# Optimization experiments

Measured on AMD Instinct MI355X. Metric: run time of the kernel, lower is better.

Reference implementation:

```python
import jax, jax.numpy as jnp
import numpy as np

T, B, D, H = 512, 64, 512, 512


def lstm_cell(x, h, c, Wih, Whh, bih, bhh):
    # PyTorch LSTMCell: gates = x @ Wih.T + h @ Whh.T + bih + bhh, order [i, f, g, o]
    gates = x @ Wih.T + h @ Whh.T + (bih + bhh)
    i, f, g, o = jnp.split(gates, 4, axis=-1)
    i = jax.nn.sigmoid(i)
    f = jax.nn.sigmoid(f)
    g = jnp.tanh(g)
    o = jax.nn.sigmoid(o)
    c_new = f * c + i * g
    h_new = o * jnp.tanh(c_new)
    return h_new, c_new


def setup_inputs() -> dict:
    key = jax.random.key(0)
    ks = jax.random.split(key, 10)
    scale = 1.0 / np.sqrt(H)
    x_data = jax.random.normal(ks[0], (T, B, D), dtype=jnp.float32)
    # realistic padding mask: sorted lengths per batch element (mask[t, b] = t < len_b)
    lengths = jax.random.randint(ks[1], (B,), T // 2, T + 1)
    x_mask = (jnp.arange(T)[:, None] < lengths[None, :]).astype(jnp.float32)
    def unif(k, shape):
        return jax.random.uniform(k, shape, jnp.float32, -scale, scale)
    params = {
        'Wih_f': unif(ks[2], (4 * H, D)), 'Whh_f': unif(ks[3], (4 * H, H)),
        'bih_f': unif(ks[4], (4 * H,)),   'bhh_f': unif(ks[5], (4 * H,)),
        'Wih_r': unif(ks[6], (4 * H, D)), 'Whh_r': unif(ks[7], (4 * H, H)),
        'bih_r': unif(ks[8], (4 * H,)),   'bhh_r': unif(ks[9], (4 * H,)),
    }
    return {'x_data': x_data, 'x_mask': x_mask, **params}


def reference(x_data, x_mask, Wih_f, Whh_f, bih_f, bhh_f, Wih_r, Whh_r, bih_r, bhh_r):
    # x_data: [T, B, D], x_mask: [T, B]
    x_rev = x_data[::-1]
    m_rev = x_mask[::-1]

    def step(carry, inp):
        hf, cf, hr, cr = carry
        xf, xr, mf, mr = inp
        hf2, cf2 = lstm_cell(xf, hf, cf, Wih_f, Whh_f, bih_f, bhh_f)
        hr2, cr2 = lstm_cell(xr, hr, cr, Wih_r, Whh_r, bih_r, bhh_r)
        mf_ = mf[:, None]
        mr_ = mr[:, None]
        hf = hf2 * mf_ + hf * (1.0 - mf_)
        cf = cf2 * mf_ + cf * (1.0 - mf_)
        hr = hr2 * mr_ + hr * (1.0 - mr_)
        cr = cr2 * mr_ + cr * (1.0 - mr_)
        return (hf, cf, hr, cr), (hf, hr)

    z = jnp.zeros((B, H), dtype=x_data.dtype)
    _, (out_f, out_r) = jax.lax.scan(step, (z, z, z, z), (x_data, x_rev, x_mask, m_rev))
    # reverse outputs of the backward direction (original inserts at front)
    return jnp.concatenate([out_f, out_r[::-1]], axis=2)  # [T, B, 2H]
```

## Files before the change

### kernel.cpp

```cpp
#include <hip/hip_runtime.h>
#include <hip/hip_cooperative_groups.h>
#include <math.h>

namespace cg = cooperative_groups;

namespace {
constexpr int T = 512, B = 64, D = 512, H = 512;
constexpr int WROW = 1028;
constexpr int CHK  = 128;
constexpr int XROW = 132;
constexpr int WLDS = 16 * WROW;
constexpr int XLDS = 2 * B * XROW;
constexpr int PROW = 36;
}

__global__ __launch_bounds__(512, 2) void bilstm_persistent(
    const float* __restrict__ x, const float* __restrict__ mask,
    const float* __restrict__ WihF, const float* __restrict__ WhhF,
    const float* __restrict__ bihF, const float* __restrict__ bhhF,
    const float* __restrict__ WihR, const float* __restrict__ WhhR,
    const float* __restrict__ bihR, const float* __restrict__ bhhR,
    float* __restrict__ hbuf, float* __restrict__ out)
{
  cg::grid_group grid = cg::this_grid();
  __shared__ float smem[WLDS + XLDS];
  float* const wlds = smem;
  float* const xh   = smem + WLDS;
  float* const P    = smem + WLDS;

  const int tid = threadIdx.x;
  const int dir = (int)blockIdx.x >> 7;
  const int j0  = ((int)blockIdx.x & 127) * 4;

  const float* __restrict__ Wih = dir ? WihR : WihF;
  const float* __restrict__ Whh = dir ? WhhR : WhhF;
  const float* __restrict__ bih = dir ? bihR : bihF;
  const float* __restrict__ bhh = dir ? bhhR : bhhF;

  for (int idx = tid; idx < 16 * 256; idx += 512) {
    const int row = idx >> 8, f4 = idx & 255;
    const int g = row >> 2, jj = row & 3;
    const int k = f4 * 4;
    const float* src = (k < D)
        ? Wih + (size_t)(g * H + j0 + jj) * D + k
        : Whh + (size_t)(g * H + j0 + jj) * H + (k - D);
    *(float4*)&wlds[row * WROW + k] = *(const float4*)src;
  }

  const int fb = tid & 63, fjj = tid >> 6;
  float bs0 = 0.f, bs1 = 0.f, bs2 = 0.f, bs3 = 0.f, cReg = 0.f, hReg = 0.f;
  if (tid < 256) {
    bs0 = bih[0 * H + j0 + fjj] + bhh[0 * H + j0 + fjj];
    bs1 = bih[1 * H + j0 + fjj] + bhh[1 * H + j0 + fjj];
    bs2 = bih[2 * H + j0 + fjj] + bhh[2 * H + j0 + fjj];
    bs3 = bih[3 * H + j0 + fjj] + bhh[3 * H + j0 + fjj];
    hbuf[((size_t)dir * B + fb) * H + j0 + fjj] = 0.f;
  }

  const int bq  = tid & 15;
  const int jjc = (tid >> 4) & 3;
  const int kq  = tid >> 6;

  float4 gx0, gx1, gx2, gx3;
  const int sb = tid >> 5, sf4 = tid & 31;

  auto issue_chunk = [&](int c, int s) {
    const int t = dir ? (T - 1 - s) : s;
    const float* src = (c < 4)
        ? x + (size_t)t * B * D + c * CHK
        : hbuf + ((size_t)((s & 1) * 2 + dir) * B) * H + (c * CHK - D);
    src += (size_t)sb * 512 + sf4 * 4;
    gx0 = *(const float4*)(src);
    gx1 = *(const float4*)(src + 16 * 512);
    gx2 = *(const float4*)(src + 32 * 512);
    gx3 = *(const float4*)(src + 48 * 512);
  };
  auto write_chunk = [&](int c) {
    float* dst = xh + (c & 1) * (B * XROW) + sb * XROW + sf4 * 4;
    *(float4*)(dst)             = gx0;
    *(float4*)(dst + 16 * XROW) = gx1;
    *(float4*)(dst + 32 * XROW) = gx2;
    *(float4*)(dst + 48 * XROW) = gx3;
  };

  issue_chunk(0, 0);
  grid.sync();

  for (int s = 0; s < T; ++s) {
    float acc[4][4];
    #pragma unroll
    for (int i = 0; i < 4; ++i)
      #pragma unroll
      for (int g = 0; g < 4; ++g) acc[i][g] = 0.f;

    #pragma unroll 2
    for (int c = 0; c < 8; ++c) {
      __syncthreads();
      write_chunk(c);
      if (c < 7) issue_chunk(c + 1, s);
      __syncthreads();
      const float* wb = wlds + jjc * WROW + c * CHK + kq * 16;
      const float* xb = xh + (c & 1) * (B * XROW) + kq * 16;
      #pragma unroll
      for (int k4 = 0; k4 < 4; ++k4) {
        const int ko = k4 * 4;
        float4 w0 = *(const float4*)(wb + 0 * 4 * WROW + ko);
        float4 w1 = *(const float4*)(wb + 1 * 4 * WROW + ko);
        float4 w2 = *(const float4*)(wb + 2 * 4 * WROW + ko);
        float4 w3 = *(const float4*)(wb + 3 * 4 * WROW + ko);
        #pragma unroll
        for (int i = 0; i < 4; ++i) {
          float4 hv = *(const float4*)(xb + (bq + 16 * i) * XROW + ko);
          acc[i][0] += hv.x * w0.x + hv.y * w0.y + hv.z * w0.z + hv.w * w0.w;
          acc[i][1] += hv.x * w1.x + hv.y * w1.y + hv.z * w1.z + hv.w * w1.w;
          acc[i][2] += hv.x * w2.x + hv.y * w2.y + hv.z * w2.z + hv.w * w2.w;
          acc[i][3] += hv.x * w3.x + hv.y * w3.y + hv.z * w3.z + hv.w * w3.w;
        }
      }
    }

    __syncthreads();
    #pragma unroll
    for (int i = 0; i < 4; ++i)
      #pragma unroll
      for (int g = 0; g < 4; ++g)
        P[((bq + 16 * i) * 4 + jjc) * PROW + g * 8 + kq] = acc[i][g];
    __syncthreads();

    if (tid < 256) {
      const float* pr = P + (fb * 4 + fjj) * PROW;
      float s0 = bs0, s1 = bs1, s2 = bs2, s3 = bs3;
      #pragma unroll
      for (int g4 = 0; g4 < 2; ++g4) {
        float4 a0 = *(const float4*)(pr + 0 * 8 + g4 * 4);
        float4 a1 = *(const float4*)(pr + 1 * 8 + g4 * 4);
        float4 a2 = *(const float4*)(pr + 2 * 8 + g4 * 4);
        float4 a3 = *(const float4*)(pr + 3 * 8 + g4 * 4);
        s0 += a0.x + a0.y + a0.z + a0.w;
        s1 += a1.x + a1.y + a1.z + a1.w;
        s2 += a2.x + a2.y + a2.z + a2.w;
        s3 += a3.x + a3.y + a3.z + a3.w;
      }
      const int t = dir ? (T - 1 - s) : s;
      const float ig = 1.f / (1.f + expf(-s0));
      const float fg = 1.f / (1.f + expf(-s1));
      const float gg = tanhf(s2);
      const float og = 1.f / (1.f + expf(-s3));
      const float cNew = fg * cReg + ig * gg;
      const float hNew = og * tanhf(cNew);
      const float m = mask[(size_t)t * B + fb];
      hReg = hNew * m + hReg * (1.f - m);
      cReg = cNew * m + cReg * (1.f - m);
      hbuf[((size_t)(((s + 1) & 1) * 2 + dir) * B + fb) * H + j0 + fjj] = hReg;
      out[((size_t)t * B + fb) * (2 * H) + (size_t)dir * H + j0 + fjj] = hReg;
    }
    if (s + 1 < T) issue_chunk(0, s + 1);
    grid.sync();
  }
}

extern "C" void kernel_launch(void* const* d_in, const int* in_sizes, int n_in,
                              void* d_out, int out_size, void* d_ws, size_t ws_size,
                              hipStream_t stream) {
  const float* x    = (const float*)d_in[0];
  const float* mask = (const float*)d_in[1];
  const float* WihF = (const float*)d_in[2];
  const float* WhhF = (const float*)d_in[3];
  const float* bihF = (const float*)d_in[4];
  const float* bhhF = (const float*)d_in[5];
  const float* WihR = (const float*)d_in[6];
  const float* WhhR = (const float*)d_in[7];
  const float* bihR = (const float*)d_in[8];
  const float* bhhR = (const float*)d_in[9];
  float* hbuf = (float*)d_ws;
  float* outp = (float*)d_out;

  void* args[] = {(void*)&x, (void*)&mask,
                  (void*)&WihF, (void*)&WhhF, (void*)&bihF, (void*)&bhhF,
                  (void*)&WihR, (void*)&WhhR, (void*)&bihR, (void*)&bhhR,
                  (void*)&hbuf, (void*)&outp};
  hipLaunchCooperativeKernel((const void*)bilstm_persistent,
                             dim3(256), dim3(512), args, 0, stream);
}
```

Before: 22.62 ms.

## Rewrite BiLSTM step with split-bf16 MFMA, register weights, per-direction counters

```diff
diff --git a/kernel.cpp b/kernel.cpp
--- a/kernel.cpp
+++ b/kernel.cpp
@@ -1,161 +1,197 @@
 #include <hip/hip_runtime.h>
-#include <hip/hip_cooperative_groups.h>
+#include <hip/hip_bf16.h>
 #include <math.h>
 
-namespace cg = cooperative_groups;
+typedef __attribute__((ext_vector_type(8))) short bf16x8;
+typedef __attribute__((ext_vector_type(4))) float f32x4;
+typedef __attribute__((ext_vector_type(4))) unsigned u32x4;
 
 namespace {
 constexpr int T = 512, B = 64, D = 512, H = 512;
-constexpr int WROW = 1028;
-constexpr int CHK  = 128;
-constexpr int XROW = 132;
-constexpr int WLDS = 16 * WROW;
-constexpr int XLDS = 2 * B * XROW;
-constexpr int PROW = 36;
-}
-
-__global__ __launch_bounds__(512, 2) void bilstm_persistent(
+constexpr int NBLK = 128;
+constexpr int PLANE = B * H;
+constexpr int XPOFF = 4096;
+}
+
+__global__ __launch_bounds__(64) void ws_init(int* cnt) {
+  if (threadIdx.x < 16) cnt[threadIdx.x] = 0;
+}
+
+static __device__ __forceinline__ f32x4 mfma16(bf16x8 a, bf16x8 b, f32x4 c) {
+  return __builtin_amdgcn_mfma_f32_16x16x32_bf16(a, b, c, 0, 0, 0);
+}
+
+static __device__ __forceinline__ void split2(float v0, float v1,
+                                              unsigned& hi, unsigned& lo) {
+  unsigned b0 = __builtin_bit_cast(unsigned, v0);
+  unsigned b1 = __builtin_bit_cast(unsigned, v1);
+  hi = (b0 >> 16) | (b1 & 0xffff0000u);
+  float r0 = v0 - __builtin_bit_cast(float, b0 & 0xffff0000u);
+  float r1 = v1 - __builtin_bit_cast(float, b1 & 0xffff0000u);
+  lo = (__builtin_bit_cast(unsigned, r0) >> 16) |
+       (__builtin_bit_cast(unsigned, r1) & 0xffff0000u);
+}
+static __device__ __forceinline__ void split8(float4 a, float4 b,
+                                              bf16x8& hi8, bf16x8& lo8) {
+  unsigned h0, h1, h2, h3, l0, l1, l2, l3;
+  split2(a.x, a.y, h0, l0); split2(a.z, a.w, h1, l1);
+  split2(b.x, b.y, h2, l2); split2(b.z, b.w, h3, l3);
+  u32x4 uh = {h0, h1, h2, h3}, ul = {l0, l1, l2, l3};
+  hi8 = __builtin_bit_cast(bf16x8, uh);
+  lo8 = __builtin_bit_cast(bf16x8, ul);
+}
+
+__global__ __launch_bounds__(512, 2) void bilstm_mfma(
     const float* __restrict__ x, const float* __restrict__ mask,
     const float* __restrict__ WihF, const float* __restrict__ WhhF,
     const float* __restrict__ bihF, const float* __restrict__ bhhF,
     const float* __restrict__ WihR, const float* __restrict__ WhhR,
     const float* __restrict__ bihR, const float* __restrict__ bhhR,
-    float* __restrict__ hbuf, float* __restrict__ out)
+    unsigned short* __restrict__ hpl, int* __restrict__ cnt,
+    float* __restrict__ out)
 {
-  cg::grid_group grid = cg::this_grid();
-  __shared__ float smem[WLDS + XLDS];
-  float* const wlds = smem;
-  float* const xh   = smem + WLDS;
-  float* const P    = smem + WLDS;
-
-  const int tid = threadIdx.x;
-  const int dir = (int)blockIdx.x >> 7;
-  const int j0  = ((int)blockIdx.x & 127) * 4;
+  __shared__ float P[XPOFF + 2 * 4096];
+
+  const int tid  = threadIdx.x;
+  const int dir  = (int)blockIdx.x >> 7;
+  const int j0   = ((int)blockIdx.x & 127) * 4;
+  const int wave = tid >> 6, lane = tid & 63;
+  const int q = lane >> 4, ln15 = lane & 15;
+  const bool is_h = wave >= 4;
+  const int wh = wave - 4;
 
   const float* __restrict__ Wih = dir ? WihR : WihF;
   const float* __restrict__ Whh = dir ? WhhR : WhhF;
   const float* __restrict__ bih = dir ? bihR : bihF;
   const float* __restrict__ bhh = dir ? bhhR : bhhF;
 
-  for (int idx = tid; idx < 16 * 256; idx += 512) {
-    const int row = idx >> 8, f4 = idx & 255;
-    const int g = row >> 2, jj = row & 3;
-    const int k = f4 * 4;
-    const float* src = (k < D)
-        ? Wih + (size_t)(g * H + j0 + jj) * D + k
-        : Whh + (size_t)(g * H + j0 + jj) * H + (k - D);
-    *(float4*)&wlds[row * WROW + k] = *(const float4*)src;
-  }
-
-  const int fb = tid & 63, fjj = tid >> 6;
+  const int jj = ln15 >> 2, g = ln15 & 3;
+
+  bf16x8 Whi[4], Wlo[4];
+  {
+    const float* Wm  = is_h ? Whh : Wih;
+    const int kb     = (is_h ? wh : wave) * 128;
+    const float* wr  = Wm + (size_t)(g * H + j0 + jj) * 512 + kb;
+    #pragma unroll
+    for (int ks = 0; ks < 4; ++ks) {
+      const float* p = wr + ks * 32 + q * 8;
+      split8(*(const float4*)p, *(const float4*)(p + 4), Whi[ks], Wlo[ks]);
+    }
+  }
+
+  const int fb = (tid >> 2) & 63, fjj = tid & 3;
   float bs0 = 0.f, bs1 = 0.f, bs2 = 0.f, bs3 = 0.f, cReg = 0.f, hReg = 0.f;
   if (tid < 256) {
     bs0 = bih[0 * H + j0 + fjj] + bhh[0 * H + j0 + fjj];
     bs1 = bih[1 * H + j0 + fjj] + bhh[1 * H + j0 + fjj];
     bs2 = bih[2 * H + j0 + fjj] + bhh[2 * H + j0 + fjj];
     bs3 = bih[3 * H + j0 + fjj] + bhh[3 * H + j0 + fjj];
-    hbuf[((size_t)dir * B + fb) * H + j0 + fjj] = 0.f;
-  }
-
-  const int bq  = tid & 15;
-  const int jjc = (tid >> 4) & 3;
-  const int kq  = tid >> 6;
-
-  float4 gx0, gx1, gx2, gx3;
-  const int sb = tid >> 5, sf4 = tid & 31;
-
-  auto issue_chunk = [&](int c, int s) {
-    const int t = dir ? (T - 1 - s) : s;
-    const float* src = (c < 4)
-        ? x + (size_t)t * B * D + c * CHK
-        : hbuf + ((size_t)((s & 1) * 2 + dir) * B) * H + (c * CHK - D);
-    src += (size_t)sb * 512 + sf4 * 4;
-    gx0 = *(const float4*)(src);
-    gx1 = *(const float4*)(src + 16 * 512);
-    gx2 = *(const float4*)(src + 32 * 512);
-    gx3 = *(const float4*)(src + 48 * 512);
+  }
+
+  auto x_gemm = [&](int t, int par) {
+    f32x4 acc[4] = {{0,0,0,0},{0,0,0,0},{0,0,0,0},{0,0,0,0}};
+    #pragma unroll
+    for (int mt = 0; mt < 4; ++mt) {
+      const float* xr = x + ((size_t)t * B + ln15 + 16 * mt) * D + wave * 128 + q * 8;
+      #pragma unroll
+      for (int ks = 0; ks < 4; ++ks) {
+        bf16x8 Ah, Al;
+        split8(*(const float4*)(xr + ks * 32),
+               *(const float4*)(xr + ks * 32 + 4), Ah, Al);
+        acc[mt] = mfma16(Ah, Whi[ks], acc[mt]);
+        acc[mt] = mfma16(Ah, Wlo[ks], acc[mt]);
+        acc[mt] = mfma16(Al, Whi[ks], acc[mt]);
+      }
+    }
+    float* dst = P + XPOFF + par * 4096 + wave * 1024;
+    #pragma unroll
+    for (int mt = 0; mt < 4; ++mt)
+      #pragma unroll
+      for (int r = 0; r < 4; ++r)
+        dst[mt * 256 + (q * 4 + r) * 16 + ln15] = acc[mt][r];
   };
-  auto write_chunk = [&](int c) {
-    float* dst = xh + (c & 1) * (B * XROW) + sb * XROW + sf4 * 4;
-    *(float4*)(dst)             = gx0;
-    *(float4*)(dst + 16 * XROW) = gx1;
-    *(float4*)(dst + 32 * XROW) = gx2;
-    *(float4*)(dst + 48 * XROW) = gx3;
+
+  auto h_gemm = [&](int s) {
+    const unsigned short* phi =
+        hpl + ((size_t)((s & 1) * 2 + dir) * 2) * PLANE;
+    const unsigned short* plo = phi + PLANE;
+    f32x4 acc[4] = {{0,0,0,0},{0,0,0,0},{0,0,0,0},{0,0,0,0}};
+    #pragma unroll
+    for (int mt = 0; mt < 4; ++mt) {
+      const size_t base = (size_t)(ln15 + 16 * mt) * H + wh * 128 + q * 8;
+      #pragma unroll
+      for (int ks = 0; ks < 4; ++ks) {
+        bf16x8 Ah = *(const bf16x8*)(phi + base + ks * 32);
+        bf16x8 Al = *(const bf16x8*)(plo + base + ks * 32);
+        acc[mt] = mfma16(Ah, Whi[ks], acc[mt]);
+        acc[mt] = mfma16(Ah, Wlo[ks], acc[mt]);
+        acc[mt] = mfma16(Al, Whi[ks], acc[mt]);
+      }
+    }
+    float* dst = P + wh * 1024;
+    #pragma unroll
+    for (int mt = 0; mt < 4; ++mt)
+      #pragma unroll
+      for (int r = 0; r < 4; ++r)
+        dst[mt * 256 + (q * 4 + r) * 16 + ln15] = acc[mt][r];
   };
 
-  issue_chunk(0, 0);
-  grid.sync();
+  if (is_h) {
+    for (int i = tid - 256; i < 4096; i += 256) P[i] = 0.f;
+  } else {
+    x_gemm(dir ? (T - 1) : 0, 0);
+  }
 
   for (int s = 0; s < T; ++s) {
-    float acc[4][4];
-    #pragma unroll
-    for (int i = 0; i < 4; ++i)
-      #pragma unroll
-      for (int g = 0; g < 4; ++g) acc[i][g] = 0.f;
-
-    #pragma unroll 2
-    for (int c = 0; c < 8; ++c) {
-      __syncthreads();
-      write_chunk(c);
-      if (c < 7) issue_chunk(c + 1, s);
-      __syncthreads();
-      const float* wb = wlds + jjc * WROW + c * CHK + kq * 16;
-      const float* xb = xh + (c & 1) * (B * XROW) + kq * 16;
-      #pragma unroll
-      for (int k4 = 0; k4 < 4; ++k4) {
-        const int ko = k4 * 4;
-        float4 w0 = *(const float4*)(wb + 0 * 4 * WROW + ko);
-        float4 w1 = *(const float4*)(wb + 1 * 4 * WROW + ko);
-        float4 w2 = *(const float4*)(wb + 2 * 4 * WROW + ko);
-        float4 w3 = *(const float4*)(wb + 3 * 4 * WROW + ko);
-        #pragma unroll
-        for (int i = 0; i < 4; ++i) {
-          float4 hv = *(const float4*)(xb + (bq + 16 * i) * XROW + ko);
-          acc[i][0] += hv.x * w0.x + hv.y * w0.y + hv.z * w0.z + hv.w * w0.w;
-          acc[i][1] += hv.x * w1.x + hv.y * w1.y + hv.z * w1.z + hv.w * w1.w;
-          acc[i][2] += hv.x * w2.x + hv.y * w2.y + hv.z * w2.z + hv.w * w2.w;
-          acc[i][3] += hv.x * w3.x + hv.y * w3.y + hv.z * w3.z + hv.w * w3.w;
-        }
-      }
-    }
-
+    if (is_h) {
+      if (s > 0) {
+        const int target = NBLK * s;
+        while (__hip_atomic_load(&cnt[dir], __ATOMIC_RELAXED,
+                                 __HIP_MEMORY_SCOPE_AGENT) < target)
+          __builtin_amdgcn_s_sleep(2);
+        __threadfence();
+        h_gemm(s);
+      }
+    } else {
+      if (s + 1 < T) x_gemm(dir ? (T - 2 - s) : (s + 1), (s + 1) & 1);
+    }
     __syncthreads();
-    #pragma unroll
-    for (int i = 0; i < 4; ++i)
-      #pragma unroll
-      for (int g = 0; g < 4; ++g)
-        P[((bq + 16 * i) * 4 + jjc) * PROW + g * 8 + kq] = acc[i][g];
-    __syncthreads();
 
     if (tid < 256) {
-      const float* pr = P + (fb * 4 + fjj) * PROW;
-      float s0 = bs0, s1 = bs1, s2 = bs2, s3 = bs3;
-      #pragma unroll
-      for (int g4 = 0; g4 < 2; ++g4) {
-        float4 a0 = *(const float4*)(pr + 0 * 8 + g4 * 4);
-        float4 a1 = *(const float4*)(pr + 1 * 8 + g4 * 4);
-        float4 a2 = *(const float4*)(pr + 2 * 8 + g4 * 4);
-        float4 a3 = *(const float4*)(pr + 3 * 8 + g4 * 4);
-        s0 += a0.x + a0.y + a0.z + a0.w;
-        s1 += a1.x + a1.y + a1.z + a1.w;
-        s2 += a2.x + a2.y + a2.z + a2.w;
-        s3 += a3.x + a3.y + a3.z + a3.w;
-      }
       const int t = dir ? (T - 1 - s) : s;
-      const float ig = 1.f / (1.f + expf(-s0));
-      const float fg = 1.f / (1.f + expf(-s1));
-      const float gg = tanhf(s2);
-      const float og = 1.f / (1.f + expf(-s3));
+      const float mval = mask[(size_t)t * B + fb];
+      const int off = (fb >> 4) * 256 + (fb & 15) * 16 + fjj * 4;
+      const float* xPr = P + XPOFF + (s & 1) * 4096;
+      f32x4 sum = {bs0, bs1, bs2, bs3};
+      #pragma unroll
+      for (int w = 0; w < 4; ++w) {
+        sum += *(const f32x4*)(P + w * 1024 + off);
+        sum += *(const f32x4*)(xPr + w * 1024 + off);
+      }
+      const float ig = 1.f / (1.f + expf(-sum[0]));
+      const float fg = 1.f / (1.f + expf(-sum[1]));
+      const float gg = tanhf(sum[2]);
+      const float og = 1.f / (1.f + expf(-sum[3]));
       const float cNew = fg * cReg + ig * gg;
       const float hNew = og * tanhf(cNew);
-      const float m = mask[(size_t)t * B + fb];
-      hReg = hNew * m + hReg * (1.f - m);
-      cReg = cNew * m + cReg * (1.f - m);
-      hbuf[((size_t)(((s + 1) & 1) * 2 + dir) * B + fb) * H + j0 + fjj] = hReg;
+      hReg = hNew * mval + hReg * (1.f - mval);
+      cReg = cNew * mval + cReg * (1.f - mval);
+
+      unsigned hb = __builtin_bit_cast(unsigned, hReg);
+      unsigned short hhi = (unsigned short)(hb >> 16);
+      float rres = hReg - __builtin_bit_cast(float, hb & 0xffff0000u);
+      unsigned short hlo =
+          (unsigned short)(__builtin_bit_cast(unsigned, rres) >> 16);
+      unsigned short* nh =
+          hpl + ((size_t)((((s + 1) & 1) * 2 + dir)) * 2) * PLANE +
+          (size_t)fb * H + j0 + fjj;
+      nh[0] = hhi;
+      nh[PLANE] = hlo;
       out[((size_t)t * B + fb) * (2 * H) + (size_t)dir * H + j0 + fjj] = hReg;
-    }
-    if (s + 1 < T) issue_chunk(0, s + 1);
-    grid.sync();
+      __threadfence();
+    }
+    __syncthreads();
+    if (tid == 0 && s + 1 < T) atomicAdd(&cnt[dir], 1);
   }
 }
 
@@ -172,13 +208,17 @@
   const float* WhhR = (const float*)d_in[7];
   const float* bihR = (const float*)d_in[8];
   const float* bhhR = (const float*)d_in[9];
-  float* hbuf = (float*)d_ws;
   float* outp = (float*)d_out;
+
+  int* cnt = (int*)d_ws;
+  unsigned short* hpl = (unsigned short*)((char*)d_ws + 64);
+
+  ws_init<<<1, 64, 0, stream>>>(cnt);
 
   void* args[] = {(void*)&x, (void*)&mask,
                   (void*)&WihF, (void*)&WhhF, (void*)&bihF, (void*)&bhhF,
                   (void*)&WihR, (void*)&WhhR, (void*)&bihR, (void*)&bhhR,
-                  (void*)&hbuf, (void*)&outp};
-  hipLaunchCooperativeKernel((const void*)bilstm_persistent,
+                  (void*)&hpl, (void*)&cnt, (void*)&outp};
+  hipLaunchCooperativeKernel((const void*)bilstm_mfma,
                              dim3(256), dim3(512), args, 0, stream);
 }
```

New measurement: 37.17 ms. +64.4%, slower.
